# Kernel optimization log

Measured on AMD Instinct MI355X. Metric: run time of the kernel, lower is better.

Reference implementation:

```python
import jax, jax.numpy as jnp
import numpy as np

# Static config (must match init_kwargs)
IMG_H, IMG_W = 48, 160
BEV_H, BEV_W = 128, 128
X_MIN, X_MAX, Y_MIN, Y_MAX = -51.2, 51.2, -51.2, 51.2
RES_X = (X_MAX - X_MIN) / BEV_W
RES_Y = (Y_MAX - Y_MIN) / BEV_H
C, D, B = 128, 64, 2


def setup_inputs() -> dict:
    key = jax.random.key(0)
    k1, k2, k3, k4 = jax.random.split(key, 4)
    img_features = jax.random.normal(k1, (B, C, IMG_H, IMG_W), dtype=jnp.float32)
    # depth distribution per pixel (softmax over D, as a depth net would emit)
    depth_probs = jax.nn.softmax(jax.random.normal(k2, (B, D, IMG_H, IMG_W), dtype=jnp.float32), axis=1)
    # depth bin centers: 1m .. 60m
    depth_values = jnp.linspace(1.0, 60.0, D, dtype=jnp.float32)
    # realistic pinhole intrinsics (feature-map scale) with tiny per-cam jitter
    fx, fy, cx, cy = 120.0, 120.0, IMG_W / 2.0, IMG_H / 2.0
    K0 = jnp.array([[fx, 0.0, cx], [0.0, fy, cy], [0.0, 0.0, 1.0]], dtype=jnp.float32)
    K = K0[None] + 0.01 * jax.random.normal(k3, (B, 3, 3), dtype=jnp.float32) * jnp.array(
        [[1.0, 0.0, 1.0], [0.0, 1.0, 1.0], [0.0, 0.0, 0.0]], dtype=jnp.float32)
    # cam->lidar extrinsic: cam z (forward) -> lidar x, cam x -> -lidar y, cam y -> -lidar z
    R0 = jnp.array([[0.0, 0.0, 1.0], [-1.0, 0.0, 0.0], [0.0, -1.0, 0.0]], dtype=jnp.float32)
    t0 = jnp.array([1.5, 0.0, 1.8], dtype=jnp.float32)
    T0 = jnp.eye(4, dtype=jnp.float32).at[:3, :3].set(R0).at[:3, 3].set(t0)
    T = T0[None] + jnp.zeros((B, 4, 4), dtype=jnp.float32)
    T = T.at[:, :3, 3].add(0.05 * jax.random.normal(k4, (B, 3), dtype=jnp.float32))
    return {"img_features": img_features, "depth_probs": depth_probs,
            "depth_values": depth_values, "K": K, "T": T}


def _lss_forward(img_features, depth_probs, depth_values, K, T):
    Bn, Cn, H, W = img_features.shape
    Dn = depth_values.shape[0]
    # homogeneous pixel grid [H, W, 3]
    gx, gy = jnp.meshgrid(jnp.arange(W, dtype=jnp.float32),
                          jnp.arange(H, dtype=jnp.float32), indexing="xy")
    grid = jnp.stack([gx, gy, jnp.ones_like(gx)], axis=-1)
    # unproject: rays [B, H, W, 3]
    K_inv = jnp.linalg.inv(K)
    rays = jnp.einsum("bij,hwj->bhwi", K_inv, grid)
    # points in camera frame [B, D, H, W, 3]
    pts_cam = depth_values[None, :, None, None, None] * rays[:, None]
    # camera -> lidar
    pts = jnp.einsum("bij,bdhwj->bdhwi", T[:, :3, :3], pts_cam) + T[:, None, None, None, :3, 3]
    x, y, z = pts[..., 0], pts[..., 1], pts[..., 2]
    # torch .long() truncates toward zero -> astype int32 matches
    bx = ((x - X_MIN) / RES_X).astype(jnp.int32)
    by = ((y - Y_MIN) / RES_Y).astype(jnp.int32)
    valid = (bx >= 0) & (bx < BEV_W) & (by >= 0) & (by < BEV_H) & (z > 0)
    # depth-weighted features [B, D, H, W, C], masked instead of gathered
    weighted = jnp.einsum("bchw,bdhw->bdhwc", img_features, depth_probs)
    weighted = weighted * valid[..., None]
    idx = jnp.where(valid, by * BEV_W + bx, 0).reshape(Bn, -1)
    feats = weighted.reshape(Bn, -1, Cn)
    bev_flat = jax.vmap(lambda f, i: jax.ops.segment_sum(f, i, num_segments=BEV_H * BEV_W))(feats, idx)
    return bev_flat.reshape(Bn, BEV_H, BEV_W, Cn).transpose(0, 3, 1, 2)


def reference(img_features, depth_probs, depth_values, K, T):
    return _lss_forward(img_features, depth_probs, depth_values, K, T)
```

## Files before the change

kernel.cpp:

```cpp
#include <hip/hip_runtime.h>

constexpr int IMG_H = 48, IMG_W = 160;
constexpr int HW    = IMG_H * IMG_W;
constexpr int BEV_H = 128, BEV_W = 128;
constexpr int NCELL = BEV_H * BEV_W;
constexpr int C_DIM = 128, D_DIM = 64, B_DIM = 2;
constexpr int NCELL_TOT = B_DIM * NCELL;
constexpr int NPIX_TOT  = B_DIM * HW;
constexpr int NPTS      = NPIX_TOT * D_DIM;
constexpr int MAX_ENTRIES = NPTS;
constexpr int CHUNK = 64;
constexpr int WAVES_PER_BLK = 4;
constexpr int NSHARD = 16;
constexpr int CNT_BLOCKS = NPTS / 256;
constexpr int TRN_BLOCKS = (HW / 32) * (C_DIM / 32) * B_DIM;
constexpr int PREP_TOTAL = CNT_BLOCKS + TRN_BLOCKS;
constexpr int SCAN_BLOCKS = NCELL_TOT / 256;
constexpr float X_MIN = -51.2f, Y_MIN = -51.2f;
constexpr float RES_X = 102.4f / 128.0f;
constexpr float RES_Y = 102.4f / 128.0f;

typedef _Float16 half2v __attribute__((ext_vector_type(2)));

constexpr size_t WS_IMG_T = 0;
constexpr size_t WS_TOT   = WS_IMG_T + (size_t)B_DIM * HW * C_DIM / 2;
constexpr size_t WS_HIST2 = WS_TOT + 4;
constexpr size_t WS_OUT_T = WS_HIST2 + (size_t)NSHARD * NCELL_TOT;
constexpr size_t WS_OFFS  = WS_OUT_T + (size_t)NCELL_TOT * C_DIM;
constexpr size_t WS_EKEY  = WS_OFFS + NCELL_TOT + 4;
constexpr size_t WS_EW16  = WS_EKEY + MAX_ENTRIES;
constexpr size_t MEMSET_WORDS = 4 + (size_t)NSHARD * NCELL_TOT;
constexpr int OUT_T_F4 = NCELL_TOT * C_DIM / 4;

__device__ inline int point_shard(int tid) {
    return ((tid >> 2) + (tid >> 8)) & (NSHARD - 1);
}

__device__ inline void make_ray(const float* __restrict__ K, int b, float gx, float gy,
                                float& rx, float& ry, float& rz) {
    const float* Kb = K + b * 9;
    const float a00 = Kb[0], a01 = Kb[1], a02 = Kb[2];
    const float a10 = Kb[3], a11 = Kb[4], a12 = Kb[5];
    const float a20 = Kb[6], a21 = Kb[7], a22 = Kb[8];
    const float det = a00 * (a11 * a22 - a12 * a21)
                    - a01 * (a10 * a22 - a12 * a20)
                    + a02 * (a10 * a21 - a11 * a20);
    const float inv = 1.0f / det;
    const float i00 =  (a11 * a22 - a12 * a21) * inv;
    const float i01 = -(a01 * a22 - a02 * a21) * inv;
    const float i02 =  (a01 * a12 - a02 * a11) * inv;
    const float i10 = -(a10 * a22 - a12 * a20) * inv;
    const float i11 =  (a00 * a22 - a02 * a20) * inv;
    const float i12 = -(a00 * a12 - a02 * a10) * inv;
    const float i20 =  (a10 * a21 - a11 * a20) * inv;
    const float i21 = -(a00 * a21 - a01 * a20) * inv;
    const float i22 =  (a00 * a11 - a01 * a10) * inv;
    rx = i00 * gx + i01 * gy + i02;
    ry = i10 * gx + i11 * gy + i12;
    rz = i20 * gx + i21 * gy + i22;
}

__device__ inline int point_gcell(int tid, const float* __restrict__ dv,
                                  const float* __restrict__ K,
                                  const float* __restrict__ T) {
    const int pix = tid % HW;
    const int bd  = tid / HW;
    const int d   = bd % D_DIM;
    const int b   = bd / D_DIM;
    const int h = pix / IMG_W, w = pix % IMG_W;
    float rx, ry, rz;
    make_ray(K, b, (float)w, (float)h, rx, ry, rz);
    const float* Tb = T + b * 16;
    const float dep = dv[d];
    const float px = dep * rx, py = dep * ry, pz = dep * rz;
    const float x = Tb[0] * px + Tb[1] * py + Tb[2]  * pz + Tb[3];
    const float y = Tb[4] * px + Tb[5] * py + Tb[6]  * pz + Tb[7];
    const float z = Tb[8] * px + Tb[9] * py + Tb[10] * pz + Tb[11];
    const int bx = (int)((x - X_MIN) / RES_X);
    const int by = (int)((y - Y_MIN) / RES_Y);
    const bool valid = (bx >= 0) && (bx < BEV_W) && (by >= 0) && (by < BEV_H) && (z > 0.0f);
    return valid ? (b * NCELL + by * BEV_W + bx) : -1;
}

__device__ inline bool wave_runs(int gcell, int lane, int& run_len, int& leader_idx) {
    const int left = __shfl_up(gcell, 1);
    const bool is_leader = (lane == 0) || (left != gcell);
    const unsigned long long lmask = __ballot(is_leader);
    const unsigned long long rest = (lane == 63) ? 0ULL : (lmask >> (lane + 1));
    const int f = __ffsll((unsigned long long)rest);
    run_len = f ? f : (64 - lane);
    const unsigned long long below =
        lmask & ((lane == 63) ? ~0ULL : ((1ULL << (lane + 1)) - 1ULL));
    leader_idx = 63 - __clzll((long long)below);
    return is_leader;
}

__global__ __launch_bounds__(256) void k_prep(const float* __restrict__ img,
                                              _Float16* __restrict__ img_t,
                                              const float* __restrict__ dv,
                                              const float* __restrict__ K,
                                              const float* __restrict__ T,
                                              int* __restrict__ hist2,
                                              float4* __restrict__ out_t4) {
    __shared__ float tile[32][33];
    const int t = threadIdx.x;

    {
        const int i = blockIdx.x * 256 + t;
        if (i < OUT_T_F4) out_t4[i] = make_float4(0.f, 0.f, 0.f, 0.f);
    }

    if (blockIdx.x < CNT_BLOCKS) {
        const int tid = blockIdx.x * 256 + t;
        const int gcell = point_gcell(tid, dv, K, T);
        const int lane = t & 63;
        int run_len, leader_idx;
        const bool lead = wave_runs(gcell, lane, run_len, leader_idx);
        if (lead && gcell >= 0)
            atomicAdd(&hist2[(size_t)point_shard(tid) * NCELL_TOT + gcell], run_len);
    } else {
        const int bi = blockIdx.x - CNT_BLOCKS;
        const int px_t = bi % (HW / 32);
        const int c_t  = (bi / (HW / 32)) % (C_DIM / 32);
        const int b    = bi / ((HW / 32) * (C_DIM / 32));
        const int tx = t & 31, ty = t >> 5;
        const int pix0 = px_t * 32, c0 = c_t * 32;
        #pragma unroll
        for (int j = 0; j < 32; j += 8)
            tile[ty + j][tx] = img[((size_t)(b * C_DIM + c0 + ty + j)) * HW + pix0 + tx];
        __syncthreads();
        #pragma unroll
        for (int j = 0; j < 32; j += 8)
            img_t[((size_t)(b * HW + pix0 + ty + j)) * C_DIM + c0 + tx] =
                (_Float16)tile[tx][ty + j];
    }
}

__global__ __launch_bounds__(256) void k_scan(int* __restrict__ hist2,
                                              int* __restrict__ offs,
                                              int* __restrict__ tot) {
    __shared__ int lds[256];
    __shared__ int s_base;
    const int b = blockIdx.x;
    const int t = threadIdx.x;
    const int cell = b * 256 + t;
    int run = 0;
    #pragma unroll
    for (int sh = 0; sh < NSHARD; ++sh) {
        const size_t idx = (size_t)sh * NCELL_TOT + cell;
        const int c = hist2[idx];
        hist2[idx] = run;
        run += c;
    }
    const int h = run;
    lds[t] = h;
    __syncthreads();
    #pragma unroll
    for (int off = 1; off < 256; off <<= 1) {
        const int v = (t >= off) ? lds[t - off] : 0;
        __syncthreads();
        lds[t] += v;
        __syncthreads();
    }
    const int incl = lds[t];
    const int S = lds[255];
    if (t == 0) {
        s_base = atomicAdd(&tot[0], S);
        const int arr = atomicAdd(&tot[1], 1);
        if (arr == SCAN_BLOCKS - 1)
            offs[NCELL_TOT] = atomicAdd(&tot[0], 0);
    }
    __syncthreads();
    offs[cell] = s_base + incl - h;
}

__global__ __launch_bounds__(256) void k_fill(const float* __restrict__ dp,
                                              const float* __restrict__ dv,
                                              const float* __restrict__ K,
                                              const float* __restrict__ T,
                                              const int* __restrict__ offs,
                                              int* __restrict__ cursor2,
                                              int* __restrict__ ekey,
                                              unsigned short* __restrict__ ew16) {
    const int tid = blockIdx.x * 256 + threadIdx.x;
    const int gcell = point_gcell(tid, dv, K, T);
    const int lane = threadIdx.x & 63;
    int run_len, leader_idx;
    const bool lead = wave_runs(gcell, lane, run_len, leader_idx);
    int base = 0;
    if (lead && gcell >= 0)
        base = offs[gcell]
             + atomicAdd(&cursor2[(size_t)point_shard(tid) * NCELL_TOT + gcell], run_len);
    base = __shfl(base, leader_idx);
    if (gcell < 0) return;
    const int slot = base + (lane - leader_idx);
    const float p = dp[tid];
    ekey[slot] = (gcell << 13) | (tid % HW);
    ew16[slot] = (unsigned short)__float2uint_rn(p * 65535.0f);
}

__global__ __launch_bounds__(256) void k_chunk_gather(
    const _Float16* __restrict__ img_t,
    const int* __restrict__ offs,
    const int* __restrict__ ekey,
    const unsigned short* __restrict__ ew16,
    float* __restrict__ out_t)
{
    const int total = offs[NCELL_TOT];
    const int wave  = threadIdx.x >> 6;
    const int lane  = threadIdx.x & 63;
    const int base  = (blockIdx.x * WAVES_PER_BLK + wave) * CHUNK;
    if (base >= total) return;

    const int eidx = min(base + lane, total - 1);
    const int   mykey = ekey[eidx];
    const float myw   = (base + lane < total)
                        ? (float)ew16[base + lane] * (1.0f / 65535.0f) : 0.0f;
    const int mywi = __float_as_int(myw);

    const int c2 = lane * 2;
    const int fc    = __builtin_amdgcn_readlane(mykey, 0) >> 13;
    const int lcell = __builtin_amdgcn_readlane(mykey, 63) >> 13;
    const bool shared_first = (base > 0) && ((ekey[base - 1] >> 13) == fc);
    const bool shared_last  = (base + CHUNK < total) && ((ekey[base + CHUNK] >> 13) == lcell);

    int prev = fc;
    float2 acc = make_float2(0.0f, 0.0f);

#define LOAD16(g, V)                                                             \
    do {                                                                         \
        _Pragma("unroll")                                                        \
        for (int k = 0; k < 16; ++k) {                                           \
            const int key = __builtin_amdgcn_readlane(mykey, (g) * 16 + k);      \
            const int pix = key & 8191;                                          \
            const int bb  = key >> 27;                                           \
            V[k] = *reinterpret_cast<const half2v*>(                             \
                &img_t[((size_t)(bb * HW + pix)) * C_DIM + c2]);                 \
        }                                                                        \
    } while (0)

#define FLUSHP(cell)                                                             \
    do {                                                                         \
        float* o = &out_t[(size_t)(cell) * C_DIM + c2];                          \
        const bool shared_ = ((cell) == fc && shared_first) ||                   \
                             ((cell) == lcell && shared_last);                   \
        if (shared_) {                                                           \
            atomicAdd(o, acc.x);                                                 \
            atomicAdd(o + 1, acc.y);                                             \
        } else {                                                                 \
            *reinterpret_cast<float2*>(o) = acc;            \
        }                                                                        \
    } while (0)

#define ACC16(g, V)                                                              \
    do {                                                                         \
        _Pragma("unroll")                                                        \
        for (int k = 0; k < 16; ++k) {                                           \
            const int   key = __builtin_amdgcn_readlane(mykey, (g) * 16 + k);    \
            const float wgt =                                                    \
                __int_as_float(__builtin_amdgcn_readlane(mywi, (g) * 16 + k));   \
            const int gcell = key >> 13;                                         \
            if (gcell != prev) {                              \
                FLUSHP(prev);                                                    \
                acc = make_float2(0.0f, 0.0f);                                   \
                prev = gcell;                                                    \
            }                                                                    \
            acc.x = fmaf((float)V[k][0], wgt, acc.x);                            \
            acc.y = fmaf((float)V[k][1], wgt, acc.y);                            \
        }                                                                        \
    } while (0)

    half2v v0[16], v1[16], v2[16], v3[16];
    LOAD16(0, v0);
    LOAD16(1, v1);
    LOAD16(2, v2);
    LOAD16(3, v3);
    ACC16(0, v0);
    ACC16(1, v1);
    ACC16(2, v2);
    ACC16(3, v3);
    FLUSHP(prev);

#undef LOAD16
#undef FLUSHP
#undef ACC16
}

__global__ __launch_bounds__(256) void k_untranspose(const float* __restrict__ out_t,
                                                     float* __restrict__ out) {
    __shared__ float tile[32][33];
    const int b = blockIdx.z;
    const int tx = threadIdx.x, ty = threadIdx.y;
    const int cell0 = blockIdx.x * 32, c0 = blockIdx.y * 32;
    const float* src = out_t + (size_t)b * NCELL * C_DIM;
    #pragma unroll
    for (int j = 0; j < 32; j += 8)
        tile[ty + j][tx] = src[((size_t)(cell0 + ty + j)) * C_DIM + c0 + tx];
    __syncthreads();
    #pragma unroll
    for (int j = 0; j < 32; j += 8)
        out[((size_t)(b * C_DIM + c0 + ty + j)) * NCELL + cell0 + tx] = tile[tx][ty + j];
}

extern "C" void kernel_launch(void* const* d_in, const int* in_sizes, int n_in,
                              void* d_out, int out_size, void* d_ws, size_t ws_size,
                              hipStream_t stream) {
    const float* img = (const float*)d_in[0];
    const float* dp  = (const float*)d_in[1];
    const float* dv  = (const float*)d_in[2];
    const float* K   = (const float*)d_in[3];
    const float* T   = (const float*)d_in[4];
    float* out = (float*)d_out;

    _Float16* img_t = (_Float16*)d_ws;
    int*   tot    = (int*)d_ws + WS_TOT;
    int*   hist2  = (int*)d_ws + WS_HIST2;
    float* out_t  = (float*)d_ws + WS_OUT_T;
    int*   offs   = (int*)d_ws + WS_OFFS;
    int*   ekey   = (int*)d_ws + WS_EKEY;
    unsigned short* ew16 = (unsigned short*)((int*)d_ws + WS_EW16);
    (void)ws_size;

    hipMemsetAsync(tot, 0, MEMSET_WORDS * sizeof(int), stream);

    k_prep<<<PREP_TOTAL, 256, 0, stream>>>(img, img_t, dv, K, T, hist2,
                                           (float4*)out_t);
    k_scan<<<SCAN_BLOCKS, 256, 0, stream>>>(hist2, offs, tot);
    k_fill<<<NPTS / 256, 256, 0, stream>>>(dp, dv, K, T, offs, hist2, ekey, ew16);
    constexpr int GATHER_BLOCKS = MAX_ENTRIES / (CHUNK * WAVES_PER_BLK);
    k_chunk_gather<<<GATHER_BLOCKS, 256, 0, stream>>>(img_t, offs, ekey, ew16, out_t);
    k_untranspose<<<dim3(NCELL / 32, C_DIM / 32, B_DIM), dim3(32, 8), 0, stream>>>(
        out_t, out);
}
```

Before: 141.5 us.

## Split gather entries per batch, stride over chunks, use nontemporal access

The scan now gives each batch its own entry region, with batch 1 starting at NPTS/2 and a separate per-batch total, so the compacted list is segmented by batch. The gather kernel alternates batches across blocks by block parity and walks chunks with a grid-stride loop instead of one chunk per wave. Entry key/weight loads and the non-shared output stores use nontemporal hints to avoid polluting cache with streaming data. The launch grid stays sized for the worst case, so many waves may still do no work, and the extra loop and index arithmetic add some overhead.

```diff
diff --git a/kernel.cpp b/kernel.cpp
--- a/kernel.cpp
+++ b/kernel.cpp
@@ -16,6 +16,7 @@
 constexpr int TRN_BLOCKS = (HW / 32) * (C_DIM / 32) * B_DIM;
 constexpr int PREP_TOTAL = CNT_BLOCKS + TRN_BLOCKS;
 constexpr int SCAN_BLOCKS = NCELL_TOT / 256;
+constexpr int GATHER_BLOCKS = MAX_ENTRIES / (CHUNK * WAVES_PER_BLK);
 constexpr float X_MIN = -51.2f, Y_MIN = -51.2f;
 constexpr float RES_X = 102.4f / 128.0f;
 constexpr float RES_Y = 102.4f / 128.0f;
@@ -144,6 +145,7 @@
     const int b = blockIdx.x;
     const int t = threadIdx.x;
     const int cell = b * 256 + t;
+    const int batch = b >> 6;
     int run = 0;
     #pragma unroll
     for (int sh = 0; sh < NSHARD; ++sh) {
@@ -165,10 +167,12 @@
     const int incl = lds[t];
     const int S = lds[255];
     if (t == 0) {
-        s_base = atomicAdd(&tot[0], S);
+        s_base = (batch ? NPTS / 2 : 0) + atomicAdd(&tot[batch * 2], S);
         const int arr = atomicAdd(&tot[1], 1);
-        if (arr == SCAN_BLOCKS - 1)
+        if (arr == SCAN_BLOCKS - 1) {
             offs[NCELL_TOT] = atomicAdd(&tot[0], 0);
+            offs[NCELL_TOT + 1] = atomicAdd(&tot[2], 0);
+        }
     }
     __syncthreads();
     offs[cell] = s_base + incl - h;
@@ -206,26 +210,34 @@
     const unsigned short* __restrict__ ew16,
     float* __restrict__ out_t)
 {
-    const int total = offs[NCELL_TOT];
+    const int n0 = offs[NCELL_TOT];
+    const int n1 = offs[NCELL_TOT + 1];
     const int wave  = threadIdx.x >> 6;
     const int lane  = threadIdx.x & 63;
-    const int base  = (blockIdx.x * WAVES_PER_BLK + wave) * CHUNK;
-    if (base >= total) return;
-
-    const int eidx = min(base + lane, total - 1);
-    const int   mykey = ekey[eidx];
-    const float myw   = (base + lane < total)
-                        ? (float)ew16[base + lane] * (1.0f / 65535.0f) : 0.0f;
-    const int mywi = __float_as_int(myw);
-
+    const int p     = blockIdx.x & 1;
+    const int j     = blockIdx.x >> 1;
+    const int start = p ? (NPTS / 2) : 0;
+    const int limit = start + (p ? n1 : n0);
+    const int nch   = ((p ? n1 : n0) + CHUNK - 1) >> 6;
     const int c2 = lane * 2;
-    const int fc    = __builtin_amdgcn_readlane(mykey, 0) >> 13;
-    const int lcell = __builtin_amdgcn_readlane(mykey, 63) >> 13;
-    const bool shared_first = (base > 0) && ((ekey[base - 1] >> 13) == fc);
-    const bool shared_last  = (base + CHUNK < total) && ((ekey[base + CHUNK] >> 13) == lcell);
-
-    int prev = fc;
-    float2 acc = make_float2(0.0f, 0.0f);
+
+    for (int c = (j << 2) + wave; c < nch; c += (GATHER_BLOCKS >> 1) << 2) {
+        const int base = start + c * CHUNK;
+        const int eidx = min(base + lane, limit - 1);
+        const int   mykey = __builtin_nontemporal_load(&ekey[eidx]);
+        const float myw   = (base + lane < limit)
+            ? (float)__builtin_nontemporal_load(&ew16[base + lane]) * (1.0f / 65535.0f)
+            : 0.0f;
+        const int mywi = __float_as_int(myw);
+
+        const int fc    = __builtin_amdgcn_readlane(mykey, 0) >> 13;
+        const int lcell = __builtin_amdgcn_readlane(mykey, 63) >> 13;
+        const bool shared_first = (base > start) && ((ekey[base - 1] >> 13) == fc);
+        const bool shared_last  = (base + CHUNK < limit) &&
+                                  ((ekey[base + CHUNK] >> 13) == lcell);
+
+        int prev = fc;
+        float2 acc = make_float2(0.0f, 0.0f);
 
 #define LOAD16(g, V)                                                             \
     do {                                                                         \
@@ -248,7 +260,8 @@
             atomicAdd(o, acc.x);                                                 \
             atomicAdd(o + 1, acc.y);                                             \
         } else {                                                                 \
-            *reinterpret_cast<float2*>(o) = acc;            \
+            __builtin_nontemporal_store(*reinterpret_cast<double*>(&acc),        \
+                                        reinterpret_cast<double*>(o));           \
         }                                                                        \
     } while (0)
 
@@ -270,20 +283,21 @@
         }                                                                        \
     } while (0)
 
-    half2v v0[16], v1[16], v2[16], v3[16];
-    LOAD16(0, v0);
-    LOAD16(1, v1);
-    LOAD16(2, v2);
-    LOAD16(3, v3);
-    ACC16(0, v0);
-    ACC16(1, v1);
-    ACC16(2, v2);
-    ACC16(3, v3);
-    FLUSHP(prev);
+        half2v v0[16], v1[16], v2[16], v3[16];
+        LOAD16(0, v0);
+        LOAD16(1, v1);
+        LOAD16(2, v2);
+        LOAD16(3, v3);
+        ACC16(0, v0);
+        ACC16(1, v1);
+        ACC16(2, v2);
+        ACC16(3, v3);
+        FLUSHP(prev);
 
 #undef LOAD16
 #undef FLUSHP
 #undef ACC16
+    }
 }
 
 __global__ __launch_bounds__(256) void k_untranspose(const float* __restrict__ out_t,
@@ -327,7 +341,6 @@
                                            (float4*)out_t);
     k_scan<<<SCAN_BLOCKS, 256, 0, stream>>>(hist2, offs, tot);
     k_fill<<<NPTS / 256, 256, 0, stream>>>(dp, dv, K, T, offs, hist2, ekey, ew16);
-    constexpr int GATHER_BLOCKS = MAX_ENTRIES / (CHUNK * WAVES_PER_BLK);
     k_chunk_gather<<<GATHER_BLOCKS, 256, 0, stream>>>(img_t, offs, ekey, ew16, out_t);
     k_untranspose<<<dim3(NCELL / 32, C_DIM / 32, B_DIM), dim3(32, 8), 0, stream>>>(
         out_t, out);
```

New measurement: 141.5 us. About the same (-0.0%).
